# Performance work log

Hardware: AMD Instinct MI355X
Metric: run time of the kernel (lower is better)

Reference implementation:

```python
import jax, jax.numpy as jnp
import numpy as np

NUM_HEADS = 16
BLOCK = 64  # block_size = min(64, N)

def setup_inputs() -> dict:
    key = jax.random.key(0)
    k0, k1, k2 = jax.random.split(key, 3)
    B, N, C = 2, 2048, 1024
    x = jax.random.normal(k0, (B, N, C), dtype=jnp.float32)
    w_qkv = jax.random.normal(k1, (3 * C, C), dtype=jnp.float32) * 0.02  # torch Linear weight [out,in]
    w_proj = jax.random.normal(k2, (C, C), dtype=jnp.float32) * 0.02
    b_proj = jnp.zeros((C,), dtype=jnp.float32)
    return {"x": x, "w_qkv": w_qkv, "w_proj": w_proj, "b_proj": b_proj}

def reference(x, w_qkv, w_proj, b_proj):
    B, N, C = x.shape
    H = NUM_HEADS
    hd = C // H
    bs = min(BLOCK, N)
    scale = hd ** -0.5
    # qkv projection: [B,N,3C] -> [3,B,H,N,hd]
    qkv = (x @ w_qkv.T).reshape(B, N, 3, H, hd).transpose(2, 0, 3, 1, 4)
    q, k, v = qkv[0], qkv[1], qkv[2]
    # block-causal mask: query block i attends to all key blocks <= i
    blk = jnp.arange(N) // bs
    mask = blk[:, None] >= blk[None, :]  # [N,N]
    scores = jnp.einsum('bhqd,bhkd->bhqk', q, k) * scale
    scores = jnp.where(mask, scores, -jnp.inf)
    weights = jax.nn.softmax(scores, axis=-1)
    out = jnp.einsum('bhqk,bhkd->bhqd', weights, v)
    out = out.transpose(0, 2, 1, 3).reshape(B, N, C)
    return out @ w_proj.T + b_proj
```

## Files before the change

### kernel.cpp

```cpp
#include <hip/hip_runtime.h>

typedef __attribute__((ext_vector_type(8))) short bf16x8;
typedef __attribute__((ext_vector_type(4))) float f32x4;
typedef __attribute__((ext_vector_type(2))) unsigned int u32x2;
typedef __attribute__((ext_vector_type(8))) unsigned short ushort8v;

__device__ __forceinline__ unsigned short f2bf(float f) {
  unsigned int u = __float_as_uint(f);
  u += 0x7fffu + ((u >> 16) & 1u);
  return (unsigned short)(u >> 16);
}

__device__ __forceinline__ void gload_lds16(const unsigned short* g, unsigned short* l) {
  __builtin_amdgcn_global_load_lds(
      (const __attribute__((address_space(1))) unsigned int*)g,
      (__attribute__((address_space(3))) unsigned int*)l,
      16, 0, 0);
}

__global__ void cvt_all(const float* __restrict__ x, const float* __restrict__ wq,
                        const float* __restrict__ wp, unsigned short* __restrict__ dst) {
  const int n1 = 4096 * 1024 / 8, n2 = 3072 * 1024 / 8, n3 = 1024 * 1024 / 8;
  int stride = gridDim.x * blockDim.x;
  for (int i = blockIdx.x * blockDim.x + threadIdx.x; i < n1 + n2 + n3; i += stride) {
    const float* s; int j;
    if (i < n1)           { s = x;  j = i; }
    else if (i < n1 + n2) { s = wq; j = i - n1; }
    else                  { s = wp; j = i - n1 - n2; }
    float4 a = ((const float4*)s)[j * 2];
    float4 b = ((const float4*)s)[j * 2 + 1];
    ushort8v o;
    o[0] = f2bf(a.x); o[1] = f2bf(a.y); o[2] = f2bf(a.z); o[3] = f2bf(a.w);
    o[4] = f2bf(b.x); o[5] = f2bf(b.y); o[6] = f2bf(b.z); o[7] = f2bf(b.w);
    ((ushort8v*)dst)[i] = o;
  }
}

__device__ __forceinline__ void gemm128_bt(const unsigned short* __restrict__ A,
                                           const unsigned short* __restrict__ Bt,
                                           unsigned short* As, unsigned short* Bs,
                                           int tm, int tn, f32x4 acc[4][4]) {
  const int K = 1024;
  int tid = threadIdx.x;
  int w = tid >> 6, l = tid & 63;
  int wr = w >> 1, wc = w & 1;
  int g = l >> 4, c = l & 15;

  int srow = w * 32 + (l >> 2);
  int skoff = (((l & 3) ^ ((srow >> 1) & 3)) * 8);
  const unsigned short* gA = A + (size_t)(tm * 128 + srow) * K + skoff;
  const unsigned short* gB = Bt + (size_t)(tn * 128 + srow) * K + skoff;
  unsigned short* lA = As + (w * 32) * 32;
  unsigned short* lB = Bs + (w * 32) * 32;

  int rx = (c >> 1) & 3;
  int arow = wr * 64 + c;
  int brow = wc * 64 + c;

  for (int k0 = 0; k0 < K; k0 += 32) {
    gload_lds16(gA, lA);
    gload_lds16(gA + 16 * K, lA + 16 * 32);
    gload_lds16(gB, lB);
    gload_lds16(gB + 16 * K, lB + 16 * 32);
    gA += 32; gB += 32;
    __syncthreads();
    bf16x8 af[4], bfr[4];
#pragma unroll
    for (int mi = 0; mi < 4; ++mi)
      af[mi] = *(const bf16x8*)((const char*)As + (arow + mi * 16) * 64 + ((g ^ rx) << 4));
#pragma unroll
    for (int ni = 0; ni < 4; ++ni)
      bfr[ni] = *(const bf16x8*)((const char*)Bs + (brow + ni * 16) * 64 + ((g ^ rx) << 4));
#pragma unroll
    for (int mi = 0; mi < 4; ++mi)
#pragma unroll
      for (int ni = 0; ni < 4; ++ni)
        acc[mi][ni] = __builtin_amdgcn_mfma_f32_16x16x32_bf16(af[mi], bfr[ni], acc[mi][ni], 0, 0, 0);
    __syncthreads();
  }
}

__global__ __launch_bounds__(256) void qkv_gemm(const unsigned short* __restrict__ xb,
                                                const unsigned short* __restrict__ wb,
                                                unsigned short* __restrict__ Qp,
                                                unsigned short* __restrict__ Kp,
                                                unsigned short* __restrict__ Vt) {
  __shared__ unsigned short As[128 * 32];
  __shared__ unsigned short Bs[128 * 32];
  f32x4 acc[4][4];
#pragma unroll
  for (int i = 0; i < 4; ++i)
#pragma unroll
    for (int j = 0; j < 4; ++j) acc[i][j] = f32x4{0.f, 0.f, 0.f, 0.f};
  int id = (blockIdx.x & 7) * 96 + (blockIdx.x >> 3);
  int tm = id / 24, tn = id % 24;
  gemm128_bt(xb, wb, As, Bs, tm, tn, acc);

  int tid = threadIdx.x;
  int w = tid >> 6, l = tid & 63;
  int wr = w >> 1, wc = w & 1;
  int g = l >> 4, c = l & 15;
  const float QSCALE = 0.125f * 1.44269504088896f;
#pragma unroll
  for (int mi = 0; mi < 4; ++mi)
#pragma unroll
    for (int ni = 0; ni < 4; ++ni)
#pragma unroll
      for (int r = 0; r < 4; ++r) {
        int row = tm * 128 + wr * 64 + mi * 16 + g * 4 + r;
        int col = tn * 128 + wc * 64 + ni * 16 + c;
        int b = row >> 11, seq = row & 2047;
        int t = col >> 10;
        int h = (col >> 6) & 15, d = col & 63;
        size_t bh = (size_t)b * 16 + h;
        float v = acc[mi][ni][r];
        if (t == 0)      Qp[(bh * 2048 + seq) * 64 + d] = f2bf(v * QSCALE);
        else if (t == 1) Kp[(bh * 2048 + seq) * 64 + d] = f2bf(v);
        else             Vt[(bh * 64 + d) * 2048 + seq] = f2bf(v);
      }
}

__global__ __launch_bounds__(256, 3) void attn_fa(const unsigned short* __restrict__ Qp,
                                                  const unsigned short* __restrict__ Kp,
                                                  const unsigned short* __restrict__ Vt,
                                                  unsigned short* __restrict__ attn) {
  __shared__ unsigned short Ks[2][4096];
  __shared__ unsigned short Vs[2][4096];
  int tid = threadIdx.x;
  int w = tid >> 6, l = tid & 63;
  int g = l >> 4, c = l & 15;

  int idx = blockIdx.x;
  int pos = idx >> 3;
  int qb = 31 - (pos >> 2);
  int bh = (idx & 7) + 8 * (pos & 3);

  const unsigned short* Qbh = Qp + (size_t)bh * 2048 * 64;
  const unsigned short* Kbh = Kp + (size_t)bh * 2048 * 64;
  const unsigned short* Vbh = Vt + (size_t)bh * 64 * 2048;

  int rowA, colA, rowB, colB;
  { int L = tid * 16;         int P = L ^ (((L >> 7) & 7) << 4); rowA = P >> 7; colA = (P & 127) >> 1; }
  { int L = (tid + 256) * 16; int P = L ^ (((L >> 7) & 7) << 4); rowB = P >> 7; colB = (P & 127) >> 1; }
  const unsigned short* gKA = Kbh + rowA * 64 + colA;
  const unsigned short* gKB = Kbh + rowB * 64 + colB;
  const unsigned short* gVA = Vbh + (size_t)rowA * 2048 + colA;
  const unsigned short* gVB = Vbh + (size_t)rowB * 2048 + colB;

#define STAGE(buf, kb)                                              \
  do {                                                              \
    gload_lds16(gKA + (kb) * 4096, &Ks[(buf)][w * 512]);            \
    gload_lds16(gKB + (kb) * 4096, &Ks[(buf)][w * 512 + 2048]);     \
    gload_lds16(gVA + (kb) * 64,  &Vs[(buf)][w * 512]);             \
    gload_lds16(gVB + (kb) * 64,  &Vs[(buf)][w * 512 + 2048]);      \
  } while (0)

  bf16x8 qf[4][2];
#pragma unroll
  for (int qg = 0; qg < 4; ++qg) {
    size_t qrow = (size_t)qb * 64 + qg * 16 + c;
    qf[qg][0] = *(const bf16x8*)(Qbh + qrow * 64 + 8 * g);
    qf[qg][1] = *(const bf16x8*)(Qbh + qrow * 64 + 32 + 8 * g);
  }

  float lp4[4] = {0.f, 0.f, 0.f, 0.f};
  f32x4 o[4][4];
#pragma unroll
  for (int qg = 0; qg < 4; ++qg)
#pragma unroll
    for (int df = 0; df < 4; ++df) o[qg][df] = f32x4{0.f, 0.f, 0.f, 0.f};

  int xorv = c & 7;
  int krow = w * 16 + c;

  int cur = 0;
  STAGE(0, 0);
  __syncthreads();
  for (int kb = 0; kb <= qb; ++kb) {
    if (kb < qb) STAGE(1 - cur, kb + 1);

    const char* Kb = (const char*)&Ks[cur][0];
    const char* Vb = (const char*)&Vs[cur][0];
    bf16x8 kf0 = *(const bf16x8*)(Kb + krow * 128 + (((0 * 4 + g) ^ xorv) * 16));
    bf16x8 kf1 = *(const bf16x8*)(Kb + krow * 128 + (((1 * 4 + g) ^ xorv) * 16));
    u32x2 vf[4];
#pragma unroll
    for (int df = 0; df < 4; ++df)
      vf[df] = *(const u32x2*)(Vb + (df * 16 + c) * 128 + (((2 * w + (g >> 1)) ^ xorv) * 16) + 8 * (g & 1));
    u32x2 pa[4];
#pragma unroll
    for (int qg = 0; qg < 4; ++qg) {
      f32x4 s4 = f32x4{0.f, 0.f, 0.f, 0.f};
      s4 = __builtin_amdgcn_mfma_f32_16x16x32_bf16(kf0, qf[qg][0], s4, 0, 0, 0);
      s4 = __builtin_amdgcn_mfma_f32_16x16x32_bf16(kf1, qf[qg][1], s4, 0, 0, 0);
      float p0 = __builtin_amdgcn_exp2f(s4[0]);
      float p1 = __builtin_amdgcn_exp2f(s4[1]);
      float p2 = __builtin_amdgcn_exp2f(s4[2]);
      float p3 = __builtin_amdgcn_exp2f(s4[3]);
      lp4[qg] += (p0 + p1) + (p2 + p3);
      unsigned int w0, w1;
      asm("v_cvt_pk_bf16_f32 %0, %1, %2" : "=v"(w0) : "v"(p0), "v"(p1));
      asm("v_cvt_pk_bf16_f32 %0, %1, %2" : "=v"(w1) : "v"(p2), "v"(p3));
      pa[qg][0] = w0; pa[qg][1] = w1;
    }
#pragma unroll
    for (int qg = 0; qg < 4; ++qg)
#pragma unroll
      for (int df = 0; df < 4; ++df)
        asm("v_mfma_f32_16x16x16_bf16 %0, %1, %2, %0"
            : "+v"(o[qg][df]) : "v"(pa[qg]), "v"(vf[df]));
    __syncthreads();
    cur ^= 1;
  }
#undef STAGE

  float* Ored  = (float*)&Ks[0][0];
  float* lpred = (float*)&Vs[0][0];

  float lpw[4];
#pragma unroll
  for (int qg = 0; qg < 4; ++qg) {
    float v = lp4[qg];
    v += __shfl_xor(v, 16);
    v += __shfl_xor(v, 32);
    lpw[qg] = v;
  }
  if (g == 0) {
#pragma unroll
    for (int qg = 0; qg < 4; ++qg) lpred[w * 64 + qg * 16 + c] = lpw[qg];
  }
  for (int ww = 0; ww < 4; ++ww) {
    if (w == ww) {
#pragma unroll
      for (int qg = 0; qg < 4; ++qg)
#pragma unroll
        for (int df = 0; df < 4; ++df)
#pragma unroll
          for (int r = 0; r < 4; ++r) {
            int q = qg * 16 + 4 * g + r, d = df * 16 + c;
            if (ww == 0) Ored[q * 64 + d] = o[qg][df][r];
            else         Ored[q * 64 + d] += o[qg][df][r];
          }
    }
    __syncthreads();
  }

  float inv[4];
#pragma unroll
  for (int r = 0; r < 4; ++r) {
    int q = w * 16 + g * 4 + r;
    float s = (lpred[q] + lpred[64 + q]) + (lpred[128 + q] + lpred[192 + q]);
    inv[r] = __builtin_amdgcn_rcpf(s);
  }
  int b = bh >> 4, h = bh & 15;
#pragma unroll
  for (int df = 0; df < 4; ++df)
#pragma unroll
    for (int r = 0; r < 4; ++r) {
      int q = w * 16 + g * 4 + r;
      int row = qb * 64 + q;
      int colc = h * 64 + df * 16 + c;
      attn[((size_t)b * 2048 + row) * 1024 + colc] = f2bf(Ored[q * 64 + df * 16 + c] * inv[r]);
    }
}

__global__ __launch_bounds__(256) void proj_gemm(const unsigned short* __restrict__ attn,
                                                 const unsigned short* __restrict__ wpb,
                                                 const float* __restrict__ bias,
                                                 float* __restrict__ out) {
  __shared__ unsigned short As[128 * 32];
  __shared__ unsigned short Bs[128 * 32];
  f32x4 acc[4][4];
#pragma unroll
  for (int i = 0; i < 4; ++i)
#pragma unroll
    for (int j = 0; j < 4; ++j) acc[i][j] = f32x4{0.f, 0.f, 0.f, 0.f};
  int id = (blockIdx.x & 7) * 32 + (blockIdx.x >> 3);
  int tm = id / 8, tn = id % 8;
  gemm128_bt(attn, wpb, As, Bs, tm, tn, acc);

  int tid = threadIdx.x;
  int w = tid >> 6, l = tid & 63;
  int wr = w >> 1, wc = w & 1;
  int g = l >> 4, c = l & 15;
#pragma unroll
  for (int mi = 0; mi < 4; ++mi)
#pragma unroll
    for (int ni = 0; ni < 4; ++ni)
#pragma unroll
      for (int r = 0; r < 4; ++r) {
        int row = tm * 128 + wr * 64 + mi * 16 + g * 4 + r;
        int col = tn * 128 + wc * 64 + ni * 16 + c;
        out[(size_t)row * 1024 + col] = acc[mi][ni][r] + bias[col];
      }
}

extern "C" void kernel_launch(void* const* d_in, const int* in_sizes, int n_in,
                              void* d_out, int out_size, void* d_ws, size_t ws_size,
                              hipStream_t stream) {
  (void)in_sizes; (void)n_in; (void)out_size; (void)ws_size;
  const float* x      = (const float*)d_in[0];
  const float* w_qkv  = (const float*)d_in[1];
  const float* w_proj = (const float*)d_in[2];
  const float* b_proj = (const float*)d_in[3];
  float* out = (float*)d_out;

  unsigned short* xb    = (unsigned short*)d_ws;
  unsigned short* wqkvb = xb + 4096 * 1024;
  unsigned short* wpb   = wqkvb + 3072 * 1024;
  unsigned short* Qp    = wpb + 1024 * 1024;
  unsigned short* Kp    = Qp + 32 * 2048 * 64;
  unsigned short* Vt    = Kp + 32 * 2048 * 64;
  unsigned short* attn  = Vt + 32 * 64 * 2048;

  cvt_all<<<1024, 256, 0, stream>>>(x, w_qkv, w_proj, xb);
  qkv_gemm<<<768, 256, 0, stream>>>(xb, wqkvb, Qp, Kp, Vt);
  attn_fa<<<1024, 256, 0, stream>>>(Qp, Kp, Vt, attn);
  proj_gemm<<<256, 256, 0, stream>>>(attn, wpb, b_proj, out);
}
```

Measured before the change: 108.9 us.

## Shrink GEMM tiles to 128x64 with two-wave blocks for more parallelism

Replaces the 128x128 four-wave GEMM tile with a 128x64 tile computed by two waves, each owning a 64x64 sub-tile. The QKV and projection GEMMs now launch twice as many blocks, which matters most for the projection GEMM that previously had only 256 blocks on a 256-CU device. The global-to-LDS load pattern is reorganised so each thread loads four A rows and two B rows. In exchange, arithmetic intensity per block drops and the shared weight tiles are re-read more often.

```diff
diff --git a/kernel.cpp b/kernel.cpp
--- a/kernel.cpp
+++ b/kernel.cpp
@@ -36,32 +36,33 @@
   }
 }
 
-__device__ __forceinline__ void gemm128_bt(const unsigned short* __restrict__ A,
-                                           const unsigned short* __restrict__ Bt,
-                                           unsigned short* As, unsigned short* Bs,
-                                           int tm, int tn, f32x4 acc[4][4]) {
+__device__ __forceinline__ void gemm128x64_bt(const unsigned short* __restrict__ A,
+                                              const unsigned short* __restrict__ Bt,
+                                              unsigned short* As, unsigned short* Bs,
+                                              int tm, int tn, f32x4 acc[4][4]) {
   const int K = 1024;
   int tid = threadIdx.x;
   int w = tid >> 6, l = tid & 63;
-  int wr = w >> 1, wc = w & 1;
   int g = l >> 4, c = l & 15;
 
-  int srow = w * 32 + (l >> 2);
-  int skoff = (((l & 3) ^ ((srow >> 1) & 3)) * 8);
-  const unsigned short* gA = A + (size_t)(tm * 128 + srow) * K + skoff;
-  const unsigned short* gB = Bt + (size_t)(tn * 128 + srow) * K + skoff;
-  unsigned short* lA = As + (w * 32) * 32;
-  unsigned short* lB = Bs + (w * 32) * 32;
+  int r0 = tid >> 2;
+  int skoff = (((tid & 3) ^ ((r0 >> 1) & 3)) * 8);
+  const unsigned short* gA = A + (size_t)(tm * 128 + r0) * K + skoff;
+  const unsigned short* gB = Bt + (size_t)(tn * 64 + r0) * K + skoff;
+  unsigned short* lA = As + tid * 8;
+  unsigned short* lB = Bs + tid * 8;
 
   int rx = (c >> 1) & 3;
-  int arow = wr * 64 + c;
-  int brow = wc * 64 + c;
+  int arow = w * 64 + c;
+  int brow = c;
 
   for (int k0 = 0; k0 < K; k0 += 32) {
     gload_lds16(gA, lA);
-    gload_lds16(gA + 16 * K, lA + 16 * 32);
+    gload_lds16(gA + 32 * K, lA + 1024);
+    gload_lds16(gA + 64 * K, lA + 2048);
+    gload_lds16(gA + 96 * K, lA + 3072);
     gload_lds16(gB, lB);
-    gload_lds16(gB + 16 * K, lB + 16 * 32);
+    gload_lds16(gB + 32 * K, lB + 1024);
     gA += 32; gB += 32;
     __syncthreads();
     bf16x8 af[4], bfr[4];
@@ -80,25 +81,24 @@
   }
 }
 
-__global__ __launch_bounds__(256) void qkv_gemm(const unsigned short* __restrict__ xb,
+__global__ __launch_bounds__(128) void qkv_gemm(const unsigned short* __restrict__ xb,
                                                 const unsigned short* __restrict__ wb,
                                                 unsigned short* __restrict__ Qp,
                                                 unsigned short* __restrict__ Kp,
                                                 unsigned short* __restrict__ Vt) {
   __shared__ unsigned short As[128 * 32];
-  __shared__ unsigned short Bs[128 * 32];
+  __shared__ unsigned short Bs[64 * 32];
   f32x4 acc[4][4];
 #pragma unroll
   for (int i = 0; i < 4; ++i)
 #pragma unroll
     for (int j = 0; j < 4; ++j) acc[i][j] = f32x4{0.f, 0.f, 0.f, 0.f};
-  int id = (blockIdx.x & 7) * 96 + (blockIdx.x >> 3);
-  int tm = id / 24, tn = id % 24;
-  gemm128_bt(xb, wb, As, Bs, tm, tn, acc);
+  int id = (blockIdx.x & 7) * 192 + (blockIdx.x >> 3);
+  int tm = id / 48, tn = id % 48;
+  gemm128x64_bt(xb, wb, As, Bs, tm, tn, acc);
 
   int tid = threadIdx.x;
   int w = tid >> 6, l = tid & 63;
-  int wr = w >> 1, wc = w & 1;
   int g = l >> 4, c = l & 15;
   const float QSCALE = 0.125f * 1.44269504088896f;
 #pragma unroll
@@ -107,8 +107,8 @@
     for (int ni = 0; ni < 4; ++ni)
 #pragma unroll
       for (int r = 0; r < 4; ++r) {
-        int row = tm * 128 + wr * 64 + mi * 16 + g * 4 + r;
-        int col = tn * 128 + wc * 64 + ni * 16 + c;
+        int row = tm * 128 + w * 64 + mi * 16 + g * 4 + r;
+        int col = tn * 64 + ni * 16 + c;
         int b = row >> 11, seq = row & 2047;
         int t = col >> 10;
         int h = (col >> 6) & 15, d = col & 63;
@@ -181,8 +181,8 @@
 
     const char* Kb = (const char*)&Ks[cur][0];
     const char* Vb = (const char*)&Vs[cur][0];
-    bf16x8 kf0 = *(const bf16x8*)(Kb + krow * 128 + (((0 * 4 + g) ^ xorv) * 16));
-    bf16x8 kf1 = *(const bf16x8*)(Kb + krow * 128 + (((1 * 4 + g) ^ xorv) * 16));
+    bf16x8 kf0 = *(const bf16x8*)(Kb + krow * 128 + ((g ^ xorv) * 16));
+    bf16x8 kf1 = *(const bf16x8*)(Kb + krow * 128 + (((4 + g) ^ xorv) * 16));
     u32x2 vf[4];
 #pragma unroll
     for (int df = 0; df < 4; ++df)
@@ -264,24 +264,23 @@
     }
 }
 
-__global__ __launch_bounds__(256) void proj_gemm(const unsigned short* __restrict__ attn,
+__global__ __launch_bounds__(128) void proj_gemm(const unsigned short* __restrict__ attn,
                                                  const unsigned short* __restrict__ wpb,
                                                  const float* __restrict__ bias,
                                                  float* __restrict__ out) {
   __shared__ unsigned short As[128 * 32];
-  __shared__ unsigned short Bs[128 * 32];
+  __shared__ unsigned short Bs[64 * 32];
   f32x4 acc[4][4];
 #pragma unroll
   for (int i = 0; i < 4; ++i)
 #pragma unroll
     for (int j = 0; j < 4; ++j) acc[i][j] = f32x4{0.f, 0.f, 0.f, 0.f};
-  int id = (blockIdx.x & 7) * 32 + (blockIdx.x >> 3);
-  int tm = id / 8, tn = id % 8;
-  gemm128_bt(attn, wpb, As, Bs, tm, tn, acc);
+  int id = (blockIdx.x & 7) * 64 + (blockIdx.x >> 3);
+  int tm = id / 16, tn = id % 16;
+  gemm128x64_bt(attn, wpb, As, Bs, tm, tn, acc);
 
   int tid = threadIdx.x;
   int w = tid >> 6, l = tid & 63;
-  int wr = w >> 1, wc = w & 1;
   int g = l >> 4, c = l & 15;
 #pragma unroll
   for (int mi = 0; mi < 4; ++mi)
@@ -289,8 +288,8 @@
     for (int ni = 0; ni < 4; ++ni)
 #pragma unroll
       for (int r = 0; r < 4; ++r) {
-        int row = tm * 128 + wr * 64 + mi * 16 + g * 4 + r;
-        int col = tn * 128 + wc * 64 + ni * 16 + c;
+        int row = tm * 128 + w * 64 + mi * 16 + g * 4 + r;
+        int col = tn * 64 + ni * 16 + c;
         out[(size_t)row * 1024 + col] = acc[mi][ni][r] + bias[col];
       }
 }
@@ -314,7 +313,7 @@
   unsigned short* attn  = Vt + 32 * 64 * 2048;
 
   cvt_all<<<1024, 256, 0, stream>>>(x, w_qkv, w_proj, xb);
-  qkv_gemm<<<768, 256, 0, stream>>>(xb, wqkvb, Qp, Kp, Vt);
+  qkv_gemm<<<1536, 128, 0, stream>>>(xb, wqkvb, Qp, Kp, Vt);
   attn_fa<<<1024, 256, 0, stream>>>(Qp, Kp, Vt, attn);
-  proj_gemm<<<256, 256, 0, stream>>>(attn, wpb, b_proj, out);
-}
+  proj_gemm<<<512, 128, 0, stream>>>(attn, wpb, b_proj, out);
+}
```

New measurement: 116.2 us. +6.8%, slower.
